# Kernel optimization log

Hardware: AMD Instinct MI355X
Metric: run time of the kernel (lower is better)

Reference implementation:

```python
import jax, jax.numpy as jnp
import numpy as np

# config dims (see shape_source)
NO = 8        # Max_Object
NT = 32       # Max_Time
C = 512       # feat_dims
VD = 1024     # visual_dim
RD = 300      # self.nfeat (relation word-vector dim)
H = 4         # headnum
B = 8         # batch
No = NT * 2 * NO      # 512 object-graph nodes
Nr = NT * NO * NO     # 2048 relation-graph nodes


def _glorot(key, shape):
    fan_in = shape[0]
    return jax.random.normal(key, shape, dtype=jnp.float32) / np.sqrt(fan_in)


def setup_inputs() -> dict:
    key = jax.random.key(0)
    ks = jax.random.split(key, 18)
    inp = {
        "Ao": jax.random.uniform(ks[0], (B, No, No), dtype=jnp.float32),
        "srco": jax.random.normal(ks[1], (B, 1, 1, No, VD), dtype=jnp.float32),
        "Ar": jax.random.uniform(ks[2], (B, Nr, Nr), dtype=jnp.float32),
        "srcr": jax.random.normal(ks[3], (B, 1, 1, Nr, RD), dtype=jnp.float32),
        # GraphConvolution weights: gcl_o/gcl2_o and gcl_r/gcl2_r
        "Wo1": _glorot(ks[4], (VD, 1024)),
        "Wo2": _glorot(ks[5], (1024, C)),
        "Wr1": _glorot(ks[6], (RD, 1024)),
        "Wr2": _glorot(ks[7], (1024, C)),
        # MultiHeadAttention (e2n) projections
        "Wq": _glorot(ks[8], (C, C)), "bq": jnp.zeros((C,), jnp.float32),
        "Wk": _glorot(ks[9], (C, C)), "bk": jnp.zeros((C,), jnp.float32),
        "Wv": _glorot(ks[10], (C, C)), "bv": jnp.zeros((C,), jnp.float32),
        "Wp": _glorot(ks[11], (C, C)), "bp": jnp.zeros((C,), jnp.float32),
        # e2n_embed: Linear(2C -> C)
        "We": _glorot(ks[12], (2 * C, C)), "be": jnp.zeros((C,), jnp.float32),
    }
    return inp


def _gcn2(A, x, W1, W2):
    """Two stacked GraphConvolution layers with self-loops: relu((A+I) @ x @ W).
    A: (b,N,N), x: (b,N,Din). Vectorized over batch (torch code loops per-sample)."""
    eye = jnp.eye(A.shape[-1], dtype=A.dtype)
    Ah = A + eye
    h = jax.nn.relu(jnp.einsum('bij,bjd->bid', Ah, x @ W1))
    return jax.nn.relu(jnp.einsum('bij,bjd->bid', Ah, h @ W2))


def _mha(x, Wq, bq, Wk, bk, Wv, bv, Wp, bp):
    """Standard multi-head self-attention. x: (Bseg, S, C)."""
    Bs, S, _ = x.shape
    dh = C // H
    q = (x @ Wq + bq).reshape(Bs, S, H, dh)
    k = (x @ Wk + bk).reshape(Bs, S, H, dh)
    v = (x @ Wv + bv).reshape(Bs, S, H, dh)
    attn = jax.nn.softmax(jnp.einsum('bqhd,bkhd->bhqk', q, k) / np.sqrt(dh), axis=-1)
    o = jnp.einsum('bhqk,bkhd->bqhd', attn, v).reshape(Bs, S, C)
    return o @ Wp + bp


def _forward(Ao, srco, Ar, srcr, Wo1, Wo2, Wr1, Wr2,
             Wq, bq, Wk, bk, Wv, bv, Wp, bp, We, be):
    b = Ao.shape[0]
    # object-graph GCN (torch loops over batch; vectorized here)
    xo = srco[:, 0, 0, :, :VD]                       # (b, No, VD)
    srco_gcn = _gcn2(Ao, xo, Wo1, Wo2)               # (b, No, C)
    out_gcn_o = srco_gcn.reshape(b, NT, 2 * NO, C)
    # relation-graph GCN
    xr = srcr[:, 0, 0]                               # (b, Nr, RD)
    srcr_gcn = _gcn2(Ar, xr, Wr1, Wr2)               # (b, Nr, C)
    out_gcn_r = srcr_gcn.reshape(b, NT, NO * NO, C)
    # compute_e2n: segment-wise MHA over NO-token windows (torch loops over NO)
    r = out_gcn_r.reshape(b * NT, NO, NO, C)
    seg_a = r.reshape(b * NT * NO, NO, C)                      # rows of NOxNO grid
    a = _mha(seg_a, Wq, bq, Wk, bk, Wv, bv, Wp, bp).mean(axis=1)
    a = a.reshape(b * NT, NO, C)
    seg_o = jnp.swapaxes(r, 1, 2).reshape(b * NT * NO, NO, C)  # cols (permute 0,2,1,3)
    o = _mha(seg_o, Wq, bq, Wk, bk, Wv, bv, Wp, bp).mean(axis=1)
    o = o.reshape(b * NT, NO, C)
    tmp = jnp.concatenate([a, o], axis=1)                      # (b*NT, 2*NO, C)
    cat = jnp.concatenate([tmp, out_gcn_o.reshape(b * NT, 2 * NO, C)], axis=-1)
    out_e2n = cat @ We + be
    return out_e2n.reshape(b, NT, 2 * NO, C)


def reference(Ao, srco, Ar, srcr, Wo1, Wo2, Wr1, Wr2,
              Wq, bq, Wk, bk, Wv, bv, Wp, bp, We, be):
    return _forward(Ao, srco, Ar, srcr, Wo1, Wo2, Wr1, Wr2,
                    Wq, bq, Wk, bk, Wv, bv, Wp, bp, We, be)
```

## Files before the change

kernel.cpp:

```cpp
#include <hip/hip_runtime.h>
#include <hip/hip_bf16.h>


typedef __attribute__((ext_vector_type(4))) float f32x4;
typedef __attribute__((ext_vector_type(8))) short bf16x8s;

#define TILE 128
#define BKK 32
#define LDSS 40

__device__ inline void split2(float a, float b, unsigned& h, unsigned& l) {
    __hip_bfloat16 ha = __float2bfloat16(a), hb = __float2bfloat16(b);
    float ra = __bfloat162float(ha), rb = __bfloat162float(hb);
    __hip_bfloat16 la = __float2bfloat16(a - ra), lb = __float2bfloat16(b - rb);
    unsigned short uha = *(unsigned short*)&ha, uhb = *(unsigned short*)&hb;
    unsigned short ula = *(unsigned short*)&la, ulb = *(unsigned short*)&lb;
    h = (unsigned)uha | ((unsigned)uhb << 16);
    l = (unsigned)ula | ((unsigned)ulb << 16);
}

__device__ inline void splitw(float v, unsigned short& h, unsigned short& l) {
    __hip_bfloat16 hb = __float2bfloat16(v);
    __hip_bfloat16 lb = __float2bfloat16(v - __bfloat162float(hb));
    h = *(unsigned short*)&hb;
    l = *(unsigned short*)&lb;
}

__global__ __launch_bounds__(256) void gemm_asplit(
    const float* __restrict__ A, long long sA, int lda,
    const __hip_bfloat16* __restrict__ BTh, const __hip_bfloat16* __restrict__ BTl,
    long long sBT, int ldbt,
    __hip_bfloat16* __restrict__ Dh_, __hip_bfloat16* __restrict__ Dl_,
    long long sD, int ldd,
    const float* __restrict__ addN, long long sAddN, int ldaddN,
    const __hip_bfloat16* __restrict__ addTh, const __hip_bfloat16* __restrict__ addTl,
    long long sAddT, int ldaddT,
    int K, int relu)
{
    __shared__ __hip_bfloat16 Ah[TILE * LDSS], Al[TILE * LDSS];
    __shared__ __hip_bfloat16 Bh[TILE * LDSS], Bl[TILE * LDSS];

    const int tid  = threadIdx.x;
    const int lane = tid & 63;
    const int wave = tid >> 6;
    const int wm   = (wave >> 1) * 64;
    const int wn   = (wave & 1) * 64;
    const int row0 = blockIdx.y * TILE;
    const int col0 = blockIdx.x * TILE;
    const int b    = blockIdx.z;

    const float* Ab = A + (size_t)b * sA;
    const __hip_bfloat16* Bbh = BTh + (size_t)b * sBT;
    const __hip_bfloat16* Bbl = BTl + (size_t)b * sBT;

    f32x4 acc[4][4];
#pragma unroll
    for (int i = 0; i < 4; ++i)
#pragma unroll
        for (int j = 0; j < 4; ++j) acc[i][j] = (f32x4){0.f, 0.f, 0.f, 0.f};

    const int quad = lane >> 4;
    const int l16  = lane & 15;

    for (int k0 = 0; k0 < K; k0 += BKK) {
        __syncthreads();
#pragma unroll
        for (int it = 0; it < 2; ++it) {
            int task = tid + it * 256;
            int m = task >> 2, kq = task & 3;
            const float* ap = Ab + (size_t)(row0 + m) * lda + k0 + kq * 8;
            float4 v0 = *(const float4*)ap;
            float4 v1 = *(const float4*)(ap + 4);
            uint4 H, L;
            split2(v0.x, v0.y, H.x, L.x); split2(v0.z, v0.w, H.y, L.y);
            split2(v1.x, v1.y, H.z, L.z); split2(v1.z, v1.w, H.w, L.w);
            *(uint4*)(&Ah[m * LDSS + kq * 8]) = H;
            *(uint4*)(&Al[m * LDSS + kq * 8]) = L;
        }
#pragma unroll
        for (int it = 0; it < 2; ++it) {
            int task = tid + it * 256;
            int n = task >> 2, kq = task & 3;
            size_t off = (size_t)(col0 + n) * ldbt + k0 + kq * 8;
            *(uint4*)(&Bh[n * LDSS + kq * 8]) = *(const uint4*)(Bbh + off);
            *(uint4*)(&Bl[n * LDSS + kq * 8]) = *(const uint4*)(Bbl + off);
        }
        __syncthreads();

        bf16x8s ah[4], al[4], bh[4], bl[4];
#pragma unroll
        for (int mt = 0; mt < 4; ++mt) {
            int r = (wm + mt * 16 + l16) * LDSS + quad * 8;
            ah[mt] = *(const bf16x8s*)(&Ah[r]);
            al[mt] = *(const bf16x8s*)(&Al[r]);
        }
#pragma unroll
        for (int nt = 0; nt < 4; ++nt) {
            int r = (wn + nt * 16 + l16) * LDSS + quad * 8;
            bh[nt] = *(const bf16x8s*)(&Bh[r]);
            bl[nt] = *(const bf16x8s*)(&Bl[r]);
        }
#pragma unroll
        for (int mt = 0; mt < 4; ++mt)
#pragma unroll
            for (int nt = 0; nt < 4; ++nt) {
                acc[mt][nt] = __builtin_amdgcn_mfma_f32_16x16x32_bf16(ah[mt], bh[nt], acc[mt][nt], 0, 0, 0);
                acc[mt][nt] = __builtin_amdgcn_mfma_f32_16x16x32_bf16(ah[mt], bl[nt], acc[mt][nt], 0, 0, 0);
                acc[mt][nt] = __builtin_amdgcn_mfma_f32_16x16x32_bf16(al[mt], bh[nt], acc[mt][nt], 0, 0, 0);
            }
    }

    __hip_bfloat16* Dhb = Dh_ + (size_t)b * sD;
    __hip_bfloat16* Dlb = Dl_ + (size_t)b * sD;
    const float* AddN = addN ? addN + (size_t)b * sAddN : nullptr;
    const __hip_bfloat16* ATh = addTh ? addTh + (size_t)b * sAddT : nullptr;
    const __hip_bfloat16* ATl = addTl ? addTl + (size_t)b * sAddT : nullptr;
#pragma unroll
    for (int mt = 0; mt < 4; ++mt)
#pragma unroll
        for (int nt = 0; nt < 4; ++nt)
#pragma unroll
            for (int r = 0; r < 4; ++r) {
                int m = row0 + wm + mt * 16 + quad * 4 + r;
                int n = col0 + wn + nt * 16 + l16;
                float v = acc[mt][nt][r];
                if (AddN) v += AddN[(size_t)m * ldaddN + n];
                if (ATh) v += __bfloat162float(ATh[(size_t)n * ldaddT + m])
                            + __bfloat162float(ATl[(size_t)n * ldaddT + m]);
                if (relu && v < 0.f) v = 0.f;
                unsigned short hh, ll;
                splitw(v, hh, ll);
                size_t o = (size_t)m * ldd + n;
                *(unsigned short*)&Dhb[o] = hh;
                *(unsigned short*)&Dlb[o] = ll;
            }
}

__global__ __launch_bounds__(256) void gemm_planes(
    const __hip_bfloat16* __restrict__ Aph, const __hip_bfloat16* __restrict__ Apl,
    long long sA, int lda,
    const __hip_bfloat16* __restrict__ BTh, const __hip_bfloat16* __restrict__ BTl,
    long long sBT, int ldbt,
    void* __restrict__ D, __hip_bfloat16* __restrict__ Dl_, long long sD, int ldd,
    const float* __restrict__ bias,
    int K, int relu, int outMode)
{
    __shared__ __hip_bfloat16 Ah[TILE * LDSS], Al[TILE * LDSS];
    __shared__ __hip_bfloat16 Bh[TILE * LDSS], Bl[TILE * LDSS];

    const int tid  = threadIdx.x;
    const int lane = tid & 63;
    const int wave = tid >> 6;
    const int wm   = (wave >> 1) * 64;
    const int wn   = (wave & 1) * 64;
    const int row0 = blockIdx.y * TILE;
    const int col0 = blockIdx.x * TILE;
    const int b    = blockIdx.z;

    const __hip_bfloat16* Abh = Aph + (size_t)b * sA;
    const __hip_bfloat16* Abl = Apl + (size_t)b * sA;
    const __hip_bfloat16* Bbh = BTh + (size_t)b * sBT;
    const __hip_bfloat16* Bbl = BTl + (size_t)b * sBT;

    f32x4 acc[4][4];
#pragma unroll
    for (int i = 0; i < 4; ++i)
#pragma unroll
        for (int j = 0; j < 4; ++j) acc[i][j] = (f32x4){0.f, 0.f, 0.f, 0.f};

    const int quad = lane >> 4;
    const int l16  = lane & 15;

    for (int k0 = 0; k0 < K; k0 += BKK) {
        __syncthreads();
#pragma unroll
        for (int it = 0; it < 2; ++it) {
            int task = tid + it * 256;
            int m = task >> 2, kq = task & 3;
            size_t off = (size_t)(row0 + m) * lda + k0 + kq * 8;
            *(uint4*)(&Ah[m * LDSS + kq * 8]) = *(const uint4*)(Abh + off);
            *(uint4*)(&Al[m * LDSS + kq * 8]) = *(const uint4*)(Abl + off);
        }
#pragma unroll
        for (int it = 0; it < 2; ++it) {
            int task = tid + it * 256;
            int n = task >> 2, kq = task & 3;
            size_t off = (size_t)(col0 + n) * ldbt + k0 + kq * 8;
            *(uint4*)(&Bh[n * LDSS + kq * 8]) = *(const uint4*)(Bbh + off);
            *(uint4*)(&Bl[n * LDSS + kq * 8]) = *(const uint4*)(Bbl + off);
        }
        __syncthreads();

        bf16x8s ah[4], al[4], bh[4], bl[4];
#pragma unroll
        for (int mt = 0; mt < 4; ++mt) {
            int r = (wm + mt * 16 + l16) * LDSS + quad * 8;
            ah[mt] = *(const bf16x8s*)(&Ah[r]);
            al[mt] = *(const bf16x8s*)(&Al[r]);
        }
#pragma unroll
        for (int nt = 0; nt < 4; ++nt) {
            int r = (wn + nt * 16 + l16) * LDSS + quad * 8;
            bh[nt] = *(const bf16x8s*)(&Bh[r]);
            bl[nt] = *(const bf16x8s*)(&Bl[r]);
        }
#pragma unroll
        for (int mt = 0; mt < 4; ++mt)
#pragma unroll
            for (int nt = 0; nt < 4; ++nt) {
                acc[mt][nt] = __builtin_amdgcn_mfma_f32_16x16x32_bf16(ah[mt], bh[nt], acc[mt][nt], 0, 0, 0);
                acc[mt][nt] = __builtin_amdgcn_mfma_f32_16x16x32_bf16(ah[mt], bl[nt], acc[mt][nt], 0, 0, 0);
                acc[mt][nt] = __builtin_amdgcn_mfma_f32_16x16x32_bf16(al[mt], bh[nt], acc[mt][nt], 0, 0, 0);
            }
    }

    float* DbF = (float*)D + (size_t)b * sD;
    __hip_bfloat16* Dhb = (__hip_bfloat16*)D + (size_t)b * sD;
    __hip_bfloat16* Dlb = Dl_ ? Dl_ + (size_t)b * sD : nullptr;
#pragma unroll
    for (int mt = 0; mt < 4; ++mt)
#pragma unroll
        for (int nt = 0; nt < 4; ++nt)
#pragma unroll
            for (int r = 0; r < 4; ++r) {
                int m = row0 + wm + mt * 16 + quad * 4 + r;
                int n = col0 + wn + nt * 16 + l16;
                float v = acc[mt][nt][r];
                if (bias) v += bias[n];
                if (relu && v < 0.f) v = 0.f;
                if (outMode == 0) {
                    DbF[(size_t)m * ldd + n] = v;
                } else {
                    unsigned short hh, ll;
                    splitw(v, hh, ll);
                    size_t o = (size_t)m * ldd + n;
                    *(unsigned short*)&Dhb[o] = hh;
                    *(unsigned short*)&Dlb[o] = ll;
                }
            }
}

__global__ __launch_bounds__(256) void padtrans_split(
    const float* __restrict__ src,
    __hip_bfloat16* __restrict__ dsth, __hip_bfloat16* __restrict__ dstl,
    int R, int C, int Rp, int Cp)
{
    __shared__ float T[64][65];
    const int t = threadIdx.x;
    const int tr = t >> 4, tc = t & 15;
    const int c0 = blockIdx.x * 64, r0 = blockIdx.y * 64;
    const size_t bat = blockIdx.z;
    const float* sb = src + bat * (size_t)R * C;
    __hip_bfloat16* dhb = dsth + bat * (size_t)Cp * Rp;
    __hip_bfloat16* dlb = dstl + bat * (size_t)Cp * Rp;

#pragma unroll
    for (int i = 0; i < 4; ++i) {
        int rr = tr + i * 16;
        int gr = r0 + rr;
        float v0 = 0.f, v1 = 0.f, v2 = 0.f, v3 = 0.f;
        if (gr < R) {
            int c = c0 + tc * 4;
            const float* s = sb + (size_t)gr * C + c;
            if (c + 0 < C) v0 = s[0];
            if (c + 1 < C) v1 = s[1];
            if (c + 2 < C) v2 = s[2];
            if (c + 3 < C) v3 = s[3];
        }
        T[rr][tc * 4 + 0] = v0; T[rr][tc * 4 + 1] = v1;
        T[rr][tc * 4 + 2] = v2; T[rr][tc * 4 + 3] = v3;
    }
    __syncthreads();
#pragma unroll
    for (int i = 0; i < 4; ++i) {
        int cc = tr + i * 16;
        float4 v = { T[tc * 4 + 0][cc], T[tc * 4 + 1][cc],
                     T[tc * 4 + 2][cc], T[tc * 4 + 3][cc] };
        ushort4 H, L;
        splitw(v.x, H.x, L.x); splitw(v.y, H.y, L.y);
        splitw(v.z, H.z, L.z); splitw(v.w, H.w, L.w);
        size_t off = (size_t)(c0 + cc) * Rp + r0 + tc * 4;
        *(ushort4*)(dhb + off) = H;
        *(ushort4*)(dlb + off) = L;
    }
}

__global__ __launch_bounds__(256) void gemm_bf16(
    const __hip_bfloat16* __restrict__ A, long long sA, int lda,
    const __hip_bfloat16* __restrict__ B, long long sB, int ldb,
    void* __restrict__ D, long long sD, int ldd,
    const __hip_bfloat16* __restrict__ addsrc, long long sAdd, int ldadd,
    const float* __restrict__ bias,
    int K, int relu, int outF32)
{
    __shared__ __hip_bfloat16 As[TILE * LDSS];
    __shared__ __hip_bfloat16 Bs[TILE * LDSS];

    const int tid  = threadIdx.x;
    const int lane = tid & 63;
    const int wave = tid >> 6;
    const int wm   = (wave >> 1) * 64;
    const int wn   = (wave & 1) * 64;
    const int row0 = blockIdx.y * TILE;
    const int col0 = blockIdx.x * TILE;
    const int b    = blockIdx.z;

    const __hip_bfloat16* Ab = A + (size_t)b * sA;
    const __hip_bfloat16* Bb = B + (size_t)b * sB;

    f32x4 acc[4][4];
#pragma unroll
    for (int i = 0; i < 4; ++i)
#pragma unroll
        for (int j = 0; j < 4; ++j) acc[i][j] = (f32x4){0.f, 0.f, 0.f, 0.f};

    const int quad = lane >> 4;
    const int l16  = lane & 15;

    for (int k0 = 0; k0 < K; k0 += BKK) {
        __syncthreads();
#pragma unroll
        for (int it = 0; it < 2; ++it) {
            int task = tid + it * 256;
            int m = task >> 2, kq = task & 3;
            uint4 val = *(const uint4*)(Ab + (size_t)(row0 + m) * lda + k0 + kq * 8);
            *(uint4*)(&As[m * LDSS + kq * 8]) = val;
        }
#pragma unroll
        for (int it = 0; it < 2; ++it) {
            int task = tid + it * 256;
            int kk = task >> 4, n8 = task & 15;
            uint4 val = *(const uint4*)(Bb + (size_t)(k0 + kk) * ldb + col0 + n8 * 8);
            const __hip_bfloat16* v16 = (const __hip_bfloat16*)&val;
#pragma unroll
            for (int u = 0; u < 8; ++u)
                Bs[(n8 * 8 + u) * LDSS + kk] = v16[u];
        }
        __syncthreads();

        bf16x8s afrag[4], bfrag[4];
#pragma unroll
        for (int mt = 0; mt < 4; ++mt)
            afrag[mt] = *(const bf16x8s*)(&As[(wm + mt * 16 + l16) * LDSS + quad * 8]);
#pragma unroll
        for (int nt = 0; nt < 4; ++nt)
            bfrag[nt] = *(const bf16x8s*)(&Bs[(wn + nt * 16 + l16) * LDSS + quad * 8]);
#pragma unroll
        for (int mt = 0; mt < 4; ++mt)
#pragma unroll
            for (int nt = 0; nt < 4; ++nt)
                acc[mt][nt] = __builtin_amdgcn_mfma_f32_16x16x32_bf16(
                    afrag[mt], bfrag[nt], acc[mt][nt], 0, 0, 0);
    }

    __hip_bfloat16* Db16 = (__hip_bfloat16*)D + (size_t)b * sD;
    float*          DbF  = (float*)D + (size_t)b * sD;
    const __hip_bfloat16* Addb = addsrc ? addsrc + (size_t)b * sAdd : nullptr;
#pragma unroll
    for (int mt = 0; mt < 4; ++mt)
#pragma unroll
        for (int nt = 0; nt < 4; ++nt)
#pragma unroll
            for (int r = 0; r < 4; ++r) {
                int m = row0 + wm + mt * 16 + quad * 4 + r;
                int n = col0 + wn + nt * 16 + l16;
                float v = acc[mt][nt][r];
                if (Addb) v += __bfloat162float(Addb[(size_t)m * ldadd + n]);
                if (bias) v += bias[n];
                if (relu && v < 0.f) v = 0.f;
                if (outF32) DbF[(size_t)m * ldd + n] = v;
                else        Db16[(size_t)m * ldd + n] = __float2bfloat16(v);
            }
}

__global__ void convert_kernel(const float* __restrict__ src,
                               __hip_bfloat16* __restrict__ dst, int n4)
{
    int i = blockIdx.x * blockDim.x + threadIdx.x;
    if (i >= n4) return;
    float4 v = ((const float4*)src)[i];
    __hip_bfloat16 t0 = __float2bfloat16(v.x), t1 = __float2bfloat16(v.y);
    __hip_bfloat16 t2 = __float2bfloat16(v.z), t3 = __float2bfloat16(v.w);
    ushort4 o = { *(unsigned short*)&t0, *(unsigned short*)&t1,
                  *(unsigned short*)&t2, *(unsigned short*)&t3 };
    ((ushort4*)dst)[i] = o;
}

__global__ __launch_bounds__(256) void attn_kernel(
    const float* __restrict__ q,
    const float* __restrict__ k,
    const float* __restrict__ v,
    __hip_bfloat16* __restrict__ abar)
{
    __shared__ float qs[8][512], ks[8][512], vs[8][512];
    __shared__ float sc[4][8][8];
    __shared__ float wb[4][8];

    const int tid  = threadIdx.x;
    const int mode = blockIdx.y;
    const int g    = blockIdx.x >> 3;
    const int idx  = blockIdx.x & 7;
    const int rowBase = g * 64;

    for (int t = tid; t < 512; t += 256) {
        int p = t >> 6, c8 = (t & 63) * 8;
        int row = (mode == 0) ? (rowBase + idx * 8 + p) : (rowBase + p * 8 + idx);
        const float* qp = q + (size_t)row * 512 + c8;
        const float* kp = k + (size_t)row * 512 + c8;
        const float* vp = v + (size_t)row * 512 + c8;
        *(float4*)(&qs[p][c8])     = *(const float4*)(qp);
        *(float4*)(&qs[p][c8 + 4]) = *(const float4*)(qp + 4);
        *(float4*)(&ks[p][c8])     = *(const float4*)(kp);
        *(float4*)(&ks[p][c8 + 4]) = *(const float4*)(kp + 4);
        *(float4*)(&vs[p][c8])     = *(const float4*)(vp);
        *(float4*)(&vs[p][c8 + 4]) = *(const float4*)(vp + 4);
    }
    __syncthreads();

    {
        int h = tid >> 6, l = tid & 63;
        int i = l >> 3, j = l & 7;
        const float* qrow = &qs[i][h * 128];
        const float* krow = &ks[j][h * 128];
        float s = 0.f;
#pragma unroll
        for (int d = 0; d < 128; d += 4) {
            float4 qa = *(const float4*)(qrow + d);
            float4 kb = *(const float4*)(krow + d);
            s += qa.x * kb.x + qa.y * kb.y + qa.z * kb.z + qa.w * kb.w;
        }
        sc[h][i][j] = s * 0.08838834764831845f;
    }
    __syncthreads();

    if (tid < 32) {
        int h = tid >> 3, i = tid & 7;
        float mx = -1e30f;
#pragma unroll
        for (int j = 0; j < 8; ++j) mx = fmaxf(mx, sc[h][i][j]);
        float e[8], sum = 0.f;
#pragma unroll
        for (int j = 0; j < 8; ++j) { e[j] = __expf(sc[h][i][j] - mx); sum += e[j]; }
        float inv = 1.f / sum;
#pragma unroll
        for (int j = 0; j < 8; ++j) sc[h][i][j] = e[j] * inv;
    }
    __syncthreads();

    if (tid < 32) {
        int h = tid >> 3, j = tid & 7;
        float s = 0.f;
#pragma unroll
        for (int i = 0; i < 8; ++i) s += sc[h][i][j];
        wb[h][j] = s * 0.125f;
    }
    __syncthreads();

    {
        int orow = g * 16 + mode * 8 + idx;
        for (int c = tid; c < 512; c += 256) {
            int h = c >> 7;
            float o = 0.f;
#pragma unroll
            for (int j = 0; j < 8; ++j) o += wb[h][j] * vs[j][c];
            abar[(size_t)orow * 512 + c] = __float2bfloat16(o);
        }
    }
}


extern "C" void kernel_launch(void* const* d_in, const int* in_sizes, int n_in,
                              void* d_out, int out_size, void* d_ws, size_t ws_size,
                              hipStream_t stream)
{
    const float* Ao   = (const float*)d_in[0];
    const float* srco = (const float*)d_in[1];
    const float* Ar   = (const float*)d_in[2];
    const float* srcr = (const float*)d_in[3];
    const float* Wo1  = (const float*)d_in[4];
    const float* Wo2  = (const float*)d_in[5];
    const float* Wr1  = (const float*)d_in[6];
    const float* Wr2  = (const float*)d_in[7];
    const float* Wq   = (const float*)d_in[8];
    const float* bq   = (const float*)d_in[9];
    const float* Wk   = (const float*)d_in[10];
    const float* bk   = (const float*)d_in[11];
    const float* Wv   = (const float*)d_in[12];
    const float* bv   = (const float*)d_in[13];
    const float* Wp   = (const float*)d_in[14];
    const float* bp   = (const float*)d_in[15];
    const float* We   = (const float*)d_in[16];
    const float* be   = (const float*)d_in[17];
    float* out = (float*)d_out;

    char* ws = (char*)d_ws;
    const size_t R0 = 0;
    const size_t R1 = 67108864;
    const size_t R2 = 100663296;
    const size_t R3 = 134217728;
    const size_t R4 = 167772160;
    const size_t R5 = 192937984;

    __hip_bfloat16* HRh = (__hip_bfloat16*)(ws + R0);
    __hip_bfloat16* HRl = HRh + 16777216;
    float* qF   = (float*)(ws + R0);
    float* kF   = (float*)(ws + R0 + 33554432);
    float* T2Rf = (float*)(ws + R1);
    float* vF   = (float*)(ws + R1);
    __hip_bfloat16* Uh = (__hip_bfloat16*)(ws + R2);
    __hip_bfloat16* Ul = Uh + 6291456;
    __hip_bfloat16* T2RTh = (__hip_bfloat16*)(ws + R2);
    __hip_bfloat16* T2RTl = T2RTh + 8388608;
    __hip_bfloat16* GRh = (__hip_bfloat16*)(ws + R3);
    __hip_bfloat16* GRl = GRh + 8388608;
    __hip_bfloat16* XPTh = (__hip_bfloat16*)(ws + R4);
    __hip_bfloat16* XPTl = XPTh + 6291456;
    __hip_bfloat16* ABAR = (__hip_bfloat16*)(ws + R4);
    __hip_bfloat16* WPTh = (__hip_bfloat16*)(ws + R5);
    __hip_bfloat16* WPTl = WPTh + 327680;
    __hip_bfloat16* Wr2Th = (__hip_bfloat16*)(ws + R5 + 1310720);
    __hip_bfloat16* Wr2Tl = Wr2Th + 524288;
    __hip_bfloat16* WqTh = (__hip_bfloat16*)(ws + R5 + 3407872);
    __hip_bfloat16* WqTl = WqTh + 262144;
    __hip_bfloat16* WkTh = (__hip_bfloat16*)(ws + R5 + 4456448);
    __hip_bfloat16* WkTl = WkTh + 262144;
    __hip_bfloat16* WvTh = (__hip_bfloat16*)(ws + R5 + 5505024);
    __hip_bfloat16* WvTl = WvTh + 262144;

    __hip_bfloat16* TO    = (__hip_bfloat16*)(ws + R2 + 0);
    __hip_bfloat16* HO    = (__hip_bfloat16*)(ws + R2 + 8388608);
    __hip_bfloat16* T2O   = (__hip_bfloat16*)(ws + R2 + 16777216);
    __hip_bfloat16* CAT   = (__hip_bfloat16*)(ws + R2 + 20971520);
    __hip_bfloat16* srcoB = (__hip_bfloat16*)(ws + R2 + 29360128);
    __hip_bfloat16* AoB   = (__hip_bfloat16*)(ws + R2 + 37748736);
    __hip_bfloat16* Wo1B  = (__hip_bfloat16*)(ws + R2 + 41943040);
    __hip_bfloat16* Wo2B  = (__hip_bfloat16*)(ws + R2 + 44040192);
    __hip_bfloat16* WeB   = (__hip_bfloat16*)(ws + R2 + 45088768);
    __hip_bfloat16* WpB   = (__hip_bfloat16*)(ws + R2 + 46137344);

    dim3 blk(256);
    auto cvt = [&](const float* s, __hip_bfloat16* d, int n) {
        convert_kernel<<<dim3((n / 4 + 255) / 256), blk, 0, stream>>>(s, d, n / 4);
    };

    padtrans_split<<<dim3(6, 32, 8), blk, 0, stream>>>(srcr, XPTh, XPTl, 2048, 300, 2048, 384);
    padtrans_split<<<dim3(16, 5, 1), blk, 0, stream>>>(Wr1, WPTh, WPTl, 300, 1024, 320, 1024);
    padtrans_split<<<dim3(8, 16, 1), blk, 0, stream>>>(Wr2, Wr2Th, Wr2Tl, 1024, 512, 1024, 512);
    padtrans_split<<<dim3(8, 8, 1), blk, 0, stream>>>(Wq, WqTh, WqTl, 512, 512, 512, 512);
    padtrans_split<<<dim3(8, 8, 1), blk, 0, stream>>>(Wk, WkTh, WkTl, 512, 512, 512, 512);
    padtrans_split<<<dim3(8, 8, 1), blk, 0, stream>>>(Wv, WvTh, WvTl, 512, 512, 512, 512);

    gemm_asplit<<<dim3(3, 16, 8), blk, 0, stream>>>(
        Ar, 2048LL * 2048, 2048, XPTh, XPTl, 384LL * 2048, 2048,
        Uh, Ul, 2048LL * 384, 384,
        nullptr, 0, 0, XPTh, XPTl, 384LL * 2048, 2048,
        2048, 0);
    gemm_planes<<<dim3(8, 128, 1), blk, 0, stream>>>(
        Uh, Ul, 0, 384, WPTh, WPTl, 0, 320,
        HRh, HRl, 0, 1024, nullptr, 320, 1, 1);
    gemm_planes<<<dim3(4, 128, 1), blk, 0, stream>>>(
        HRh, HRl, 0, 1024, Wr2Th, Wr2Tl, 0, 1024,
        T2Rf, nullptr, 0, 512, nullptr, 1024, 0, 0);
    padtrans_split<<<dim3(8, 32, 8), blk, 0, stream>>>(T2Rf, T2RTh, T2RTl, 2048, 512, 2048, 512);
    gemm_asplit<<<dim3(4, 16, 8), blk, 0, stream>>>(
        Ar, 2048LL * 2048, 2048, T2RTh, T2RTl, 512LL * 2048, 2048,
        GRh, GRl, 2048LL * 512, 512,
        T2Rf, 2048LL * 512, 512, nullptr, nullptr, 0, 0,
        2048, 1);
    gemm_planes<<<dim3(4, 128, 1), blk, 0, stream>>>(
        GRh, GRl, 0, 512, WqTh, WqTl, 0, 512,
        qF, nullptr, 0, 512, bq, 512, 0, 0);
    gemm_planes<<<dim3(4, 128, 1), blk, 0, stream>>>(
        GRh, GRl, 0, 512, WkTh, WkTl, 0, 512,
        kF, nullptr, 0, 512, bk, 512, 0, 0);
    gemm_planes<<<dim3(4, 128, 1), blk, 0, stream>>>(
        GRh, GRl, 0, 512, WvTh, WvTl, 0, 512,
        vF, nullptr, 0, 512, bv, 512, 0, 0);
    attn_kernel<<<dim3(2048, 2), blk, 0, stream>>>(qF, kF, vF, ABAR);

    cvt(srco, srcoB, 4194304);
    cvt(Ao, AoB, 2097152);
    cvt(Wo1, Wo1B, 1048576);
    cvt(Wo2, Wo2B, 524288);
    cvt(We, WeB, 524288);
    cvt(Wp, WpB, 262144);
    gemm_bf16<<<dim3(8, 32, 1), blk, 0, stream>>>(srcoB, 0, 1024, Wo1B, 0, 1024,
        TO, 0, 1024, nullptr, 0, 0, nullptr, 1024, 0, 0);
    gemm_bf16<<<dim3(8, 4, 8), blk, 0, stream>>>(AoB, 512LL * 512, 512, TO, 512LL * 1024, 1024,
        HO, 512LL * 1024, 1024, TO, 512LL * 1024, 1024, nullptr, 512, 1, 0);
    gemm_bf16<<<dim3(4, 32, 1), blk, 0, stream>>>(HO, 0, 1024, Wo2B, 0, 512,
        T2O, 0, 512, nullptr, 0, 0, nullptr, 1024, 0, 0);
    gemm_bf16<<<dim3(4, 4, 8), blk, 0, stream>>>(AoB, 512LL * 512, 512, T2O, 512LL * 512, 512,
        (void*)(CAT + 512), 512LL * 1024, 1024, T2O, 512LL * 512, 512, nullptr, 512, 1, 0);
    gemm_bf16<<<dim3(4, 32, 1), blk, 0, stream>>>(ABAR, 0, 512, WpB, 0, 512,
        CAT, 0, 1024, nullptr, 0, 0, bp, 512, 0, 0);
    gemm_bf16<<<dim3(4, 32, 1), blk, 0, stream>>>(CAT, 0, 1024, WeB, 0, 512,
        out, 0, 512, nullptr, 0, 0, be, 1024, 0, 1);
}
```

Before: 1.203 ms.

## Prefetch GEMM tiles into registers, swizzle block order, and pre-split Ar into bf16 planes

All three GEMM kernels now load the next K-slice from global memory into registers while the current slice is being multiplied, overlapping memory latency with MFMA work. A block-index swizzle spreads consecutive workgroups across 8 groups to change cache locality. When the workspace is large enough, the Ar matrix is split once into bf16 hi/lo planes and both Ar GEMMs read those planes through gemm_planes, which gains an epilogue add path. This avoids re-splitting fp32 Ar in every tile, at the cost of an extra pass over Ar and more register pressure.

```diff
diff --git a/kernel.cpp b/kernel.cpp
--- a/kernel.cpp
+++ b/kernel.cpp
@@ -24,6 +24,18 @@
     __hip_bfloat16 lb = __float2bfloat16(v - __bfloat162float(hb));
     h = *(unsigned short*)&hb;
     l = *(unsigned short*)&lb;
+}
+
+__device__ inline void swz_block(int& bx, int& by, int& bz) {
+    int gx = gridDim.x, gy = gridDim.y;
+    int nwg = gx * gy * gridDim.z;
+    int flat = bx + gx * (by + gy * bz);
+    int cpx = nwg >> 3;
+    int w = (flat & 7) * cpx + (flat >> 3);
+    bx = w % gx;
+    int t = w / gx;
+    by = t % gy;
+    bz = t / gy;
 }
 
 __global__ __launch_bounds__(256) void gemm_asplit(
@@ -40,14 +52,17 @@
     __shared__ __hip_bfloat16 Ah[TILE * LDSS], Al[TILE * LDSS];
     __shared__ __hip_bfloat16 Bh[TILE * LDSS], Bl[TILE * LDSS];
 
+    int bx = blockIdx.x, by = blockIdx.y, bz = blockIdx.z;
+    swz_block(bx, by, bz);
+
     const int tid  = threadIdx.x;
     const int lane = tid & 63;
     const int wave = tid >> 6;
     const int wm   = (wave >> 1) * 64;
     const int wn   = (wave & 1) * 64;
-    const int row0 = blockIdx.y * TILE;
-    const int col0 = blockIdx.x * TILE;
-    const int b    = blockIdx.z;
+    const int row0 = by * TILE;
+    const int col0 = bx * TILE;
+    const int b    = bz;
 
     const float* Ab = A + (size_t)b * sA;
     const __hip_bfloat16* Bbh = BTh + (size_t)b * sBT;
@@ -62,30 +77,52 @@
     const int quad = lane >> 4;
     const int l16  = lane & 15;
 
+    const int m0  = tid >> 2,        kq0 = tid & 3;
+    const int m1  = (tid + 256) >> 2, kq1 = (tid + 256) & 3;
+
+    float4 pA0[2], pA1[2];
+    uint4  pBh[2], pBl[2];
+    {
+        const float* ap0 = Ab + (size_t)(row0 + m0) * lda + kq0 * 8;
+        const float* ap1 = Ab + (size_t)(row0 + m1) * lda + kq1 * 8;
+        pA0[0] = *(const float4*)ap0; pA1[0] = *(const float4*)(ap0 + 4);
+        pA0[1] = *(const float4*)ap1; pA1[1] = *(const float4*)(ap1 + 4);
+        size_t ob0 = (size_t)(col0 + m0) * ldbt + kq0 * 8;
+        size_t ob1 = (size_t)(col0 + m1) * ldbt + kq1 * 8;
+        pBh[0] = *(const uint4*)(Bbh + ob0); pBl[0] = *(const uint4*)(Bbl + ob0);
+        pBh[1] = *(const uint4*)(Bbh + ob1); pBl[1] = *(const uint4*)(Bbl + ob1);
+    }
+
     for (int k0 = 0; k0 < K; k0 += BKK) {
         __syncthreads();
-#pragma unroll
-        for (int it = 0; it < 2; ++it) {
-            int task = tid + it * 256;
-            int m = task >> 2, kq = task & 3;
-            const float* ap = Ab + (size_t)(row0 + m) * lda + k0 + kq * 8;
-            float4 v0 = *(const float4*)ap;
-            float4 v1 = *(const float4*)(ap + 4);
+        {
             uint4 H, L;
-            split2(v0.x, v0.y, H.x, L.x); split2(v0.z, v0.w, H.y, L.y);
-            split2(v1.x, v1.y, H.z, L.z); split2(v1.z, v1.w, H.w, L.w);
-            *(uint4*)(&Ah[m * LDSS + kq * 8]) = H;
-            *(uint4*)(&Al[m * LDSS + kq * 8]) = L;
-        }
-#pragma unroll
-        for (int it = 0; it < 2; ++it) {
-            int task = tid + it * 256;
-            int n = task >> 2, kq = task & 3;
-            size_t off = (size_t)(col0 + n) * ldbt + k0 + kq * 8;
-            *(uint4*)(&Bh[n * LDSS + kq * 8]) = *(const uint4*)(Bbh + off);
-            *(uint4*)(&Bl[n * LDSS + kq * 8]) = *(const uint4*)(Bbl + off);
+            split2(pA0[0].x, pA0[0].y, H.x, L.x); split2(pA0[0].z, pA0[0].w, H.y, L.y);
+            split2(pA1[0].x, pA1[0].y, H.z, L.z); split2(pA1[0].z, pA1[0].w, H.w, L.w);
+            *(uint4*)(&Ah[m0 * LDSS + kq0 * 8]) = H;
+            *(uint4*)(&Al[m0 * LDSS + kq0 * 8]) = L;
+            split2(pA0[1].x, pA0[1].y, H.x, L.x); split2(pA0[1].z, pA0[1].w, H.y, L.y);
+            split2(pA1[1].x, pA1[1].y, H.z, L.z); split2(pA1[1].z, pA1[1].w, H.w, L.w);
+            *(uint4*)(&Ah[m1 * LDSS + kq1 * 8]) = H;
+            *(uint4*)(&Al[m1 * LDSS + kq1 * 8]) = L;
+            *(uint4*)(&Bh[m0 * LDSS + kq0 * 8]) = pBh[0];
+            *(uint4*)(&Bl[m0 * LDSS + kq0 * 8]) = pBl[0];
+            *(uint4*)(&Bh[m1 * LDSS + kq1 * 8]) = pBh[1];
+            *(uint4*)(&Bl[m1 * LDSS + kq1 * 8]) = pBl[1];
         }
         __syncthreads();
+
+        int k1 = k0 + BKK;
+        if (k1 < K) {
+            const float* ap0 = Ab + (size_t)(row0 + m0) * lda + k1 + kq0 * 8;
+            const float* ap1 = Ab + (size_t)(row0 + m1) * lda + k1 + kq1 * 8;
+            pA0[0] = *(const float4*)ap0; pA1[0] = *(const float4*)(ap0 + 4);
+            pA0[1] = *(const float4*)ap1; pA1[1] = *(const float4*)(ap1 + 4);
+            size_t ob0 = (size_t)(col0 + m0) * ldbt + k1 + kq0 * 8;
+            size_t ob1 = (size_t)(col0 + m1) * ldbt + k1 + kq1 * 8;
+            pBh[0] = *(const uint4*)(Bbh + ob0); pBl[0] = *(const uint4*)(Bbl + ob0);
+            pBh[1] = *(const uint4*)(Bbh + ob1); pBl[1] = *(const uint4*)(Bbl + ob1);
+        }
 
         bf16x8s ah[4], al[4], bh[4], bl[4];
 #pragma unroll
@@ -142,20 +179,26 @@
     const __hip_bfloat16* __restrict__ BTh, const __hip_bfloat16* __restrict__ BTl,
     long long sBT, int ldbt,
     void* __restrict__ D, __hip_bfloat16* __restrict__ Dl_, long long sD, int ldd,
+    const float* __restrict__ addN, long long sAddN, int ldaddN,
+    const __hip_bfloat16* __restrict__ addTh, const __hip_bfloat16* __restrict__ addTl,
+    long long sAddT, int ldaddT,
     const float* __restrict__ bias,
     int K, int relu, int outMode)
 {
     __shared__ __hip_bfloat16 Ah[TILE * LDSS], Al[TILE * LDSS];
     __shared__ __hip_bfloat16 Bh[TILE * LDSS], Bl[TILE * LDSS];
 
+    int bx = blockIdx.x, by = blockIdx.y, bz = blockIdx.z;
+    swz_block(bx, by, bz);
+
     const int tid  = threadIdx.x;
     const int lane = tid & 63;
     const int wave = tid >> 6;
     const int wm   = (wave >> 1) * 64;
     const int wn   = (wave & 1) * 64;
-    const int row0 = blockIdx.y * TILE;
-    const int col0 = blockIdx.x * TILE;
-    const int b    = blockIdx.z;
+    const int row0 = by * TILE;
+    const int col0 = bx * TILE;
+    const int b    = bz;
 
     const __hip_bfloat16* Abh = Aph + (size_t)b * sA;
     const __hip_bfloat16* Abl = Apl + (size_t)b * sA;
@@ -171,25 +214,44 @@
     const int quad = lane >> 4;
     const int l16  = lane & 15;
 
+    const int m0  = tid >> 2,         kq0 = tid & 3;
+    const int m1  = (tid + 256) >> 2, kq1 = (tid + 256) & 3;
+
+    uint4 pAh[2], pAl[2], pBh[2], pBl[2];
+    {
+        size_t oa0 = (size_t)(row0 + m0) * lda + kq0 * 8;
+        size_t oa1 = (size_t)(row0 + m1) * lda + kq1 * 8;
+        pAh[0] = *(const uint4*)(Abh + oa0); pAl[0] = *(const uint4*)(Abl + oa0);
+        pAh[1] = *(const uint4*)(Abh + oa1); pAl[1] = *(const uint4*)(Abl + oa1);
+        size_t ob0 = (size_t)(col0 + m0) * ldbt + kq0 * 8;
+        size_t ob1 = (size_t)(col0 + m1) * ldbt + kq1 * 8;
+        pBh[0] = *(const uint4*)(Bbh + ob0); pBl[0] = *(const uint4*)(Bbl + ob0);
+        pBh[1] = *(const uint4*)(Bbh + ob1); pBl[1] = *(const uint4*)(Bbl + ob1);
+    }
+
     for (int k0 = 0; k0 < K; k0 += BKK) {
         __syncthreads();
-#pragma unroll
-        for (int it = 0; it < 2; ++it) {
-            int task = tid + it * 256;
-            int m = task >> 2, kq = task & 3;
-            size_t off = (size_t)(row0 + m) * lda + k0 + kq * 8;
-            *(uint4*)(&Ah[m * LDSS + kq * 8]) = *(const uint4*)(Abh + off);
-            *(uint4*)(&Al[m * LDSS + kq * 8]) = *(const uint4*)(Abl + off);
-        }
-#pragma unroll
-        for (int it = 0; it < 2; ++it) {
-            int task = tid + it * 256;
-            int n = task >> 2, kq = task & 3;
-            size_t off = (size_t)(col0 + n) * ldbt + k0 + kq * 8;
-            *(uint4*)(&Bh[n * LDSS + kq * 8]) = *(const uint4*)(Bbh + off);
-            *(uint4*)(&Bl[n * LDSS + kq * 8]) = *(const uint4*)(Bbl + off);
-        }
+        *(uint4*)(&Ah[m0 * LDSS + kq0 * 8]) = pAh[0];
+        *(uint4*)(&Al[m0 * LDSS + kq0 * 8]) = pAl[0];
+        *(uint4*)(&Ah[m1 * LDSS + kq1 * 8]) = pAh[1];
+        *(uint4*)(&Al[m1 * LDSS + kq1 * 8]) = pAl[1];
+        *(uint4*)(&Bh[m0 * LDSS + kq0 * 8]) = pBh[0];
+        *(uint4*)(&Bl[m0 * LDSS + kq0 * 8]) = pBl[0];
+        *(uint4*)(&Bh[m1 * LDSS + kq1 * 8]) = pBh[1];
+        *(uint4*)(&Bl[m1 * LDSS + kq1 * 8]) = pBl[1];
         __syncthreads();
+
+        int k1 = k0 + BKK;
+        if (k1 < K) {
+            size_t oa0 = (size_t)(row0 + m0) * lda + k1 + kq0 * 8;
+            size_t oa1 = (size_t)(row0 + m1) * lda + k1 + kq1 * 8;
+            pAh[0] = *(const uint4*)(Abh + oa0); pAl[0] = *(const uint4*)(Abl + oa0);
+            pAh[1] = *(const uint4*)(Abh + oa1); pAl[1] = *(const uint4*)(Abl + oa1);
+            size_t ob0 = (size_t)(col0 + m0) * ldbt + k1 + kq0 * 8;
+            size_t ob1 = (size_t)(col0 + m1) * ldbt + k1 + kq1 * 8;
+            pBh[0] = *(const uint4*)(Bbh + ob0); pBl[0] = *(const uint4*)(Bbl + ob0);
+            pBh[1] = *(const uint4*)(Bbh + ob1); pBl[1] = *(const uint4*)(Bbl + ob1);
+        }
 
         bf16x8s ah[4], al[4], bh[4], bl[4];
 #pragma unroll
@@ -217,6 +279,9 @@
     float* DbF = (float*)D + (size_t)b * sD;
     __hip_bfloat16* Dhb = (__hip_bfloat16*)D + (size_t)b * sD;
     __hip_bfloat16* Dlb = Dl_ ? Dl_ + (size_t)b * sD : nullptr;
+    const float* AddN = addN ? addN + (size_t)b * sAddN : nullptr;
+    const __hip_bfloat16* ATh = addTh ? addTh + (size_t)b * sAddT : nullptr;
+    const __hip_bfloat16* ATl = addTl ? addTl + (size_t)b * sAddT : nullptr;
 #pragma unroll
     for (int mt = 0; mt < 4; ++mt)
 #pragma unroll
@@ -226,6 +291,9 @@
                 int m = row0 + wm + mt * 16 + quad * 4 + r;
                 int n = col0 + wn + nt * 16 + l16;
                 float v = acc[mt][nt][r];
+                if (AddN) v += AddN[(size_t)m * ldaddN + n];
+                if (ATh) v += __bfloat162float(ATh[(size_t)n * ldaddT + m])
+                            + __bfloat162float(ATl[(size_t)n * ldaddT + m]);
                 if (bias) v += bias[n];
                 if (relu && v < 0.f) v = 0.f;
                 if (outMode == 0) {
@@ -296,14 +364,17 @@
     __shared__ __hip_bfloat16 As[TILE * LDSS];
     __shared__ __hip_bfloat16 Bs[TILE * LDSS];
 
+    int bx = blockIdx.x, by = blockIdx.y, bz = blockIdx.z;
+    swz_block(bx, by, bz);
+
     const int tid  = threadIdx.x;
     const int lane = tid & 63;
     const int wave = tid >> 6;
     const int wm   = (wave >> 1) * 64;
     const int wn   = (wave & 1) * 64;
-    const int row0 = blockIdx.y * TILE;
-    const int col0 = blockIdx.x * TILE;
-    const int b    = blockIdx.z;
+    const int row0 = by * TILE;
+    const int col0 = bx * TILE;
+    const int b    = bz;
 
     const __hip_bfloat16* Ab = A + (size_t)b * sA;
     const __hip_bfloat16* Bb = B + (size_t)b * sB;
@@ -317,26 +388,42 @@
     const int quad = lane >> 4;
     const int l16  = lane & 15;
 
+    const int am0 = tid >> 2,         akq0 = tid & 3;
+    const int am1 = (tid + 256) >> 2, akq1 = (tid + 256) & 3;
+    const int bk0 = tid >> 4,         bn0  = tid & 15;
+    const int bk1 = (tid + 256) >> 4, bn1  = (tid + 256) & 15;
+
+    uint4 pA[2], pB[2];
+    {
+        pA[0] = *(const uint4*)(Ab + (size_t)(row0 + am0) * lda + akq0 * 8);
+        pA[1] = *(const uint4*)(Ab + (size_t)(row0 + am1) * lda + akq1 * 8);
+        pB[0] = *(const uint4*)(Bb + (size_t)(bk0) * ldb + col0 + bn0 * 8);
+        pB[1] = *(const uint4*)(Bb + (size_t)(bk1) * ldb + col0 + bn1 * 8);
+    }
+
     for (int k0 = 0; k0 < K; k0 += BKK) {
         __syncthreads();
-#pragma unroll
-        for (int it = 0; it < 2; ++it) {
-            int task = tid + it * 256;
-            int m = task >> 2, kq = task & 3;
-            uint4 val = *(const uint4*)(Ab + (size_t)(row0 + m) * lda + k0 + kq * 8);
-            *(uint4*)(&As[m * LDSS + kq * 8]) = val;
-        }
-#pragma unroll
-        for (int it = 0; it < 2; ++it) {
-            int task = tid + it * 256;
-            int kk = task >> 4, n8 = task & 15;
-            uint4 val = *(const uint4*)(Bb + (size_t)(k0 + kk) * ldb + col0 + n8 * 8);
-            const __hip_bfloat16* v16 = (const __hip_bfloat16*)&val;
+        *(uint4*)(&As[am0 * LDSS + akq0 * 8]) = pA[0];
+        *(uint4*)(&As[am1 * LDSS + akq1 * 8]) = pA[1];
+        {
+            const __hip_bfloat16* v16 = (const __hip_bfloat16*)&pB[0];
 #pragma unroll
             for (int u = 0; u < 8; ++u)
-                Bs[(n8 * 8 + u) * LDSS + kk] = v16[u];
+                Bs[(bn0 * 8 + u) * LDSS + bk0] = v16[u];
+            v16 = (const __hip_bfloat16*)&pB[1];
+#pragma unroll
+            for (int u = 0; u < 8; ++u)
+                Bs[(bn1 * 8 + u) * LDSS + bk1] = v16[u];
         }
         __syncthreads();
+
+        int k1 = k0 + BKK;
+        if (k1 < K) {
+            pA[0] = *(const uint4*)(Ab + (size_t)(row0 + am0) * lda + k1 + akq0 * 8);
+            pA[1] = *(const uint4*)(Ab + (size_t)(row0 + am1) * lda + k1 + akq1 * 8);
+            pB[0] = *(const uint4*)(Bb + (size_t)(k1 + bk0) * ldb + col0 + bn0 * 8);
+            pB[1] = *(const uint4*)(Bb + (size_t)(k1 + bk1) * ldb + col0 + bn1 * 8);
+        }
 
         bf16x8s afrag[4], bfrag[4];
 #pragma unroll
@@ -384,6 +471,20 @@
     ushort4 o = { *(unsigned short*)&t0, *(unsigned short*)&t1,
                   *(unsigned short*)&t2, *(unsigned short*)&t3 };
     ((ushort4*)dst)[i] = o;
+}
+
+__global__ void split_kernel(const float* __restrict__ src,
+                             __hip_bfloat16* __restrict__ dh,
+                             __hip_bfloat16* __restrict__ dl, int n4)
+{
+    int i = blockIdx.x * blockDim.x + threadIdx.x;
+    if (i >= n4) return;
+    float4 v = ((const float4*)src)[i];
+    ushort4 H, L;
+    splitw(v.x, H.x, L.x); splitw(v.y, H.y, L.y);
+    splitw(v.z, H.z, L.z); splitw(v.w, H.w, L.w);
+    ((ushort4*)dh)[i] = H;
+    ((ushort4*)dl)[i] = L;
 }
 
 __global__ __launch_bounds__(256) void attn_kernel(
@@ -500,6 +601,7 @@
     const size_t R3 = 134217728;
     const size_t R4 = 167772160;
     const size_t R5 = 192937984;
+    const size_t R6 = 199491584;
 
     __hip_bfloat16* HRh = (__hip_bfloat16*)(ws + R0);
     __hip_bfloat16* HRl = HRh + 16777216;
@@ -526,6 +628,9 @@
     __hip_bfloat16* WkTl = WkTh + 262144;
     __hip_bfloat16* WvTh = (__hip_bfloat16*)(ws + R5 + 5505024);
     __hip_bfloat16* WvTl = WvTh + 262144;
+    __hip_bfloat16* Arh = (__hip_bfloat16*)(ws + R6);
+    __hip_bfloat16* Arl = Arh + 33554432;
+    const bool haveArPlanes = ws_size >= R6 + 2ull * 67108864ull;
 
     __hip_bfloat16* TO    = (__hip_bfloat16*)(ws + R2 + 0);
     __hip_bfloat16* HO    = (__hip_bfloat16*)(ws + R2 + 8388608);
@@ -550,32 +655,59 @@
     padtrans_split<<<dim3(8, 8, 1), blk, 0, stream>>>(Wk, WkTh, WkTl, 512, 512, 512, 512);
     padtrans_split<<<dim3(8, 8, 1), blk, 0, stream>>>(Wv, WvTh, WvTl, 512, 512, 512, 512);
 
-    gemm_asplit<<<dim3(3, 16, 8), blk, 0, stream>>>(
-        Ar, 2048LL * 2048, 2048, XPTh, XPTl, 384LL * 2048, 2048,
-        Uh, Ul, 2048LL * 384, 384,
-        nullptr, 0, 0, XPTh, XPTl, 384LL * 2048, 2048,
-        2048, 0);
+    if (haveArPlanes) {
+        split_kernel<<<dim3(32768), blk, 0, stream>>>(Ar, Arh, Arl, 8388608);
+        gemm_planes<<<dim3(3, 16, 8), blk, 0, stream>>>(
+            Arh, Arl, 2048LL * 2048, 2048, XPTh, XPTl, 384LL * 2048, 2048,
+            Uh, Ul, 2048LL * 384, 384,
+            nullptr, 0, 0, XPTh, XPTl, 384LL * 2048, 2048,
+            nullptr, 2048, 0, 1);
+    } else {
+        gemm_asplit<<<dim3(3, 16, 8), blk, 0, stream>>>(
+            Ar, 2048LL * 2048, 2048, XPTh, XPTl, 384LL * 2048, 2048,
+            Uh, Ul, 2048LL * 384, 384,
+            nullptr, 0, 0, XPTh, XPTl, 384LL * 2048, 2048,
+            2048, 0);
+    }
     gemm_planes<<<dim3(8, 128, 1), blk, 0, stream>>>(
         Uh, Ul, 0, 384, WPTh, WPTl, 0, 320,
-        HRh, HRl, 0, 1024, nullptr, 320, 1, 1);
+        HRh, HRl, 0, 1024,
+        nullptr, 0, 0, nullptr, nullptr, 0, 0,
+        nullptr, 320, 1, 1);
     gemm_planes<<<dim3(4, 128, 1), blk, 0, stream>>>(
         HRh, HRl, 0, 1024, Wr2Th, Wr2Tl, 0, 1024,
-        T2Rf, nullptr, 0, 512, nullptr, 1024, 0, 0);
+        T2Rf, nullptr, 0, 512,
+        nullptr, 0, 0, nullptr, nullptr, 0, 0,
+        nullptr, 1024, 0, 0);
     padtrans_split<<<dim3(8, 32, 8), blk, 0, stream>>>(T2Rf, T2RTh, T2RTl, 2048, 512, 2048, 512);
-    gemm_asplit<<<dim3(4, 16, 8), blk, 0, stream>>>(
-        Ar, 2048LL * 2048, 2048, T2RTh, T2RTl, 512LL * 2048, 2048,
-        GRh, GRl, 2048LL * 512, 512,
-        T2Rf, 2048LL * 512, 512, nullptr, nullptr, 0, 0,
-        2048, 1);
+    if (haveArPlanes) {
+        gemm_planes<<<dim3(4, 16, 8), blk, 0, stream>>>(
+            Arh, Arl, 2048LL * 2048, 2048, T2RTh, T2RTl, 512LL * 2048, 2048,
+            GRh, GRl, 2048LL * 512, 512,
+            T2Rf, 2048LL * 512, 512, nullptr, nullptr, 0, 0,
+            nullptr, 2048, 1, 1);
+    } else {
+        gemm_asplit<<<dim3(4, 16, 8), blk, 0, stream>>>(
+            Ar, 2048LL * 2048, 2048, T2RTh, T2RTl, 512LL * 2048, 2048,
+            GRh, GRl, 2048LL * 512, 512,
+            T2Rf, 2048LL * 512, 512, nullptr, nullptr, 0, 0,
+            2048, 1);
+    }
     gemm_planes<<<dim3(4, 128, 1), blk, 0, stream>>>(
         GRh, GRl, 0, 512, WqTh, WqTl, 0, 512,
-        qF, nullptr, 0, 512, bq, 512, 0, 0);
+        qF, nullptr, 0, 512,
+        nullptr, 0, 0, nullptr, nullptr, 0, 0,
+        bq, 512, 0, 0);
     gemm_planes<<<dim3(4, 128, 1), blk, 0, stream>>>(
         GRh, GRl, 0, 512, WkTh, WkTl, 0, 512,
-        kF, nullptr, 0, 512, bk, 512, 0, 0);
+        kF, nullptr, 0, 512,
+        nullptr, 0, 0, nullptr, nullptr, 0, 0,
+        bk, 512, 0, 0);
     gemm_planes<<<dim3(4, 128, 1), blk, 0, stream>>>(
         GRh, GRl, 0, 512, WvTh, WvTl, 0, 512,
-        vF, nullptr, 0, 512, bv, 512, 0, 0);
+        vF, nullptr, 0, 512,
+        nullptr, 0, 0, nullptr, nullptr, 0, 0,
+        bv, 512, 0, 0);
     attn_kernel<<<dim3(2048, 2), blk, 0, stream>>>(qF, kF, vF, ABAR);
 
     cvt(srco, srcoB, 4194304);
```

Result: slower. 2.022 ms (+68.1%).
